# Kernel optimization log

Measured on AMD Instinct MI355X. Metric: run time of the kernel, lower is better.

The kernel has to match this reference:

```python
import jax, jax.numpy as jnp
import numpy as np

N_NODES = 100000
N_EDGES = 3200000
D_IN = 256
D_OUT = 256


def setup_inputs() -> dict:
    key = jax.random.key(0)
    k1, k2, k3, k4, k5 = jax.random.split(key, 5)
    inputs = jax.random.normal(k1, (N_NODES, D_IN), dtype=jnp.float32)
    # Glorot-uniform init as in _glorot_init
    init_range = np.sqrt(6.0 / (D_IN + D_OUT)).astype(np.float32)
    weight = jax.random.uniform(k2, (D_IN, D_OUT), dtype=jnp.float32,
                                minval=-init_range, maxval=init_range)
    edge_src = jax.random.randint(k3, (N_EDGES,), 0, N_NODES, dtype=jnp.int32)
    edge_dst = jax.random.randint(k4, (N_EDGES,), 0, N_NODES, dtype=jnp.int32)
    # normalized adjacency values (positive, like D^-1/2 A D^-1/2 entries)
    edge_vals = jax.random.uniform(k5, (N_EDGES,), dtype=jnp.float32)
    return {"inputs": inputs, "weight": weight, "edge_src": edge_src,
            "edge_dst": edge_dst, "edge_vals": edge_vals}


def reference(inputs, weight, edge_src, edge_dst, edge_vals):
    # x = inputs @ W          : [N, D_OUT]
    x = inputs @ weight
    # SpMM: out[d] = sum_{e: dst(e)=d} vals[e] * x[src(e)]
    msgs = edge_vals[:, None] * x[edge_src]          # [E, D_OUT]
    out = jax.ops.segment_sum(msgs, edge_dst, num_segments=inputs.shape[0])
    return jax.nn.relu(out)
```

## Files before the change

kernel.cpp:

```cpp
#include <hip/hip_runtime.h>

#define N_NODES 100000
#define N_EDGES 3200000
#define DDIM 256
#define NB 1563
#define BIN_BLK 256
#define CHUNK (N_EDGES / BIN_BLK)

typedef short s16x8 __attribute__((ext_vector_type(8)));
typedef float f32x4 __attribute__((ext_vector_type(4)));

__device__ __forceinline__ unsigned short f32_to_bf16(float f) {
    union { float f; unsigned int u; } c; c.f = f;
    unsigned int u = c.u;
    unsigned int r = u + 0x7fffu + ((u >> 16) & 1u);
    return (unsigned short)(r >> 16);
}
__device__ __forceinline__ float bf16_to_f32(unsigned short h) {
    union { unsigned int u; float f; } c; c.u = ((unsigned int)h) << 16;
    return c.f;
}

__global__ __launch_bounds__(256) void prep_w(const float* __restrict__ W,
                                              unsigned short* __restrict__ Wt) {
    __shared__ float tile[32][33];
    const int tx = threadIdx.x & 31;
    const int ty = threadIdx.x >> 5;
    const int n0 = blockIdx.x * 32;
    const int k0 = blockIdx.y * 32;
    for (int i = 0; i < 32; i += 8)
        tile[ty + i][tx] = W[(size_t)(k0 + ty + i) * DDIM + n0 + tx];
    __syncthreads();
    for (int i = 0; i < 32; i += 8)
        Wt[(size_t)(n0 + ty + i) * DDIM + k0 + tx] = f32_to_bf16(tile[tx][ty + i]);
}

__global__ __launch_bounds__(256) void gemm_mfma(const float* __restrict__ A,
                                                 const unsigned short* __restrict__ Wt,
                                                 unsigned short* __restrict__ Xb) {
    __shared__ unsigned short As[64][DDIM + 8];
    const int tid = threadIdx.x;
    const int rowBase = blockIdx.x * 64;

#pragma unroll
    for (int p = 0; p < 16; ++p) {
        const int flat = p * 256 + tid;
        const int row = flat >> 6;
        const int k4 = (flat & 63) * 4;
        const int gr = rowBase + row;
        float4 v = make_float4(0.f, 0.f, 0.f, 0.f);
        if (gr < N_NODES) v = *(const float4*)&A[(size_t)gr * DDIM + k4];
        ushort4 h;
        h.x = f32_to_bf16(v.x); h.y = f32_to_bf16(v.y);
        h.z = f32_to_bf16(v.z); h.w = f32_to_bf16(v.w);
        *(ushort4*)&As[row][k4] = h;
    }
    __syncthreads();

    const int wave = tid >> 6;
    const int lane = tid & 63;
    const int lrow = lane & 15;
    const int quad = lane >> 4;
    const int cb = wave * 64;

    f32x4 acc[4][4] = {};

#pragma unroll
    for (int ks = 0; ks < 8; ++ks) {
        const int k0 = ks * 32 + quad * 8;
        s16x8 a[4], b[4];
#pragma unroll
        for (int ri = 0; ri < 4; ++ri)
            a[ri] = *(const s16x8*)&As[ri * 16 + lrow][k0];
#pragma unroll
        for (int ci = 0; ci < 4; ++ci)
            b[ci] = *(const s16x8*)&Wt[(size_t)(cb + ci * 16 + lrow) * DDIM + k0];
#pragma unroll
        for (int ri = 0; ri < 4; ++ri)
#pragma unroll
            for (int ci = 0; ci < 4; ++ci)
                acc[ri][ci] = __builtin_amdgcn_mfma_f32_16x16x32_bf16(a[ri], b[ci], acc[ri][ci], 0, 0, 0);
    }

#pragma unroll
    for (int ri = 0; ri < 4; ++ri) {
        const int r0 = rowBase + ri * 16 + quad * 4;
#pragma unroll
        for (int rr = 0; rr < 4; ++rr) {
            const int row = r0 + rr;
            if (row < N_NODES) {
#pragma unroll
                for (int ci = 0; ci < 4; ++ci)
                    Xb[(size_t)row * DDIM + cb + ci * 16 + lrow] = f32_to_bf16(acc[ri][ci][rr]);
            }
        }
    }
}

__global__ __launch_bounds__(256) void hist_coarse(const int* __restrict__ edst,
                                                   int* __restrict__ gcounts) {
    __shared__ int h[NB];
    const int tid = threadIdx.x;
    for (int i = tid; i < NB; i += 256) h[i] = 0;
    __syncthreads();
    const int lo = blockIdx.x * CHUNK;
    const int hi = lo + CHUNK;
    for (int e = lo + tid; e < hi; e += 256) atomicAdd(&h[edst[e] >> 6], 1);
    __syncthreads();
    for (int i = tid; i < NB; i += 256)
        if (h[i]) atomicAdd(&gcounts[i], h[i]);
}

__global__ __launch_bounds__(256) void scan_coarse(const int* __restrict__ gcounts,
                                                   int* __restrict__ bbase,
                                                   int* __restrict__ bcursor,
                                                   int* __restrict__ off) {
    __shared__ int part[256];
    const int t = threadIdx.x;
    const int chunk = (NB + 255) / 256;
    const int lo = t * chunk;
    const int hi = min(lo + chunk, NB);
    int s = 0;
    for (int i = lo; i < hi; ++i) s += gcounts[i];
    part[t] = s;
    __syncthreads();
    for (int d = 1; d < 256; d <<= 1) {
        int a = (t >= d) ? part[t - d] : 0;
        __syncthreads();
        part[t] += a;
        __syncthreads();
    }
    int run = part[t] - s;
    for (int i = lo; i < hi; ++i) {
        bbase[i] = run;
        bcursor[i] = run;
        run += gcounts[i];
    }
    if (t == 255) {
        bbase[NB] = run;
        off[N_NODES] = run;
    }
}

__global__ __launch_bounds__(256) void bin_coarse(const int* __restrict__ esrc,
                                                  const int* __restrict__ edst,
                                                  const float* __restrict__ evals,
                                                  int* __restrict__ bcursor,
                                                  long long* __restrict__ tmp) {
    __shared__ int h[NB];
    __shared__ int sb[NB];
    const int tid = threadIdx.x;
    for (int i = tid; i < NB; i += 256) h[i] = 0;
    __syncthreads();
    const int lo = blockIdx.x * CHUNK;
    const int hi = lo + CHUNK;
    for (int e = lo + tid; e < hi; e += 256) atomicAdd(&h[edst[e] >> 6], 1);
    __syncthreads();
    for (int i = tid; i < NB; i += 256)
        sb[i] = h[i] ? atomicAdd(&bcursor[i], h[i]) : 0;
    __syncthreads();
    for (int e = lo + tid; e < hi; e += 256) {
        const int d = edst[e];
        const int b = d >> 6;
        const int p = atomicAdd(&sb[b], 1);
        const unsigned int lo32 = (unsigned int)(esrc[e] | ((d & 63) << 17));
        const unsigned int hi32 = (unsigned int)__float_as_int(evals[e]);
        __builtin_nontemporal_store((long long)(((unsigned long long)hi32 << 32) | lo32), &tmp[p]);
    }
}

__global__ __launch_bounds__(256) void refine(const long long* __restrict__ tmp,
                                              const int* __restrict__ bbase,
                                              int* __restrict__ off,
                                              long long* __restrict__ srcval) {
    __shared__ int nh[64];
    __shared__ int nb[64];
    const int b = blockIdx.x;
    const int tid = threadIdx.x;
    const int base = bbase[b];
    const int cnt = bbase[b + 1] - base;
    const int n0 = b * 64;
    const int nn = min(64, N_NODES - n0);
    if (tid < 64) nh[tid] = 0;
    __syncthreads();
    for (int i = tid; i < cnt; i += 256) {
        const long long q = __builtin_nontemporal_load(&tmp[base + i]);
        atomicAdd(&nh[((int)(unsigned int)q) >> 17], 1);
    }
    __syncthreads();
    if (tid == 0) {
        int run = 0;
        for (int i = 0; i < 64; ++i) { nb[i] = run; run += nh[i]; }
    }
    __syncthreads();
    if (tid < nn) off[n0 + tid] = base + nb[tid];
    __syncthreads();
    for (int i = tid; i < cnt; i += 256) {
        const long long q = __builtin_nontemporal_load(&tmp[base + i]);
        const unsigned int lo32 = (unsigned int)q;
        const int dl = (int)(lo32 >> 17);
        const int p = atomicAdd(&nb[dl], 1);
        srcval[base + p] = (long long)((q & 0xFFFFFFFF00000000ull) | (lo32 & 0x1FFFF));
    }
}

__global__ __launch_bounds__(256) void spmm_gather(const unsigned short* __restrict__ xb,
                                                   const int* __restrict__ off,
                                                   const long long* __restrict__ srcval,
                                                   float* __restrict__ out) {
    const int node = blockIdx.x * 4 + (threadIdx.x >> 6);
    const int lane = threadIdx.x & 63;
    const int start = off[node];
    const int end = off[node + 1];

    float4 acc = make_float4(0.f, 0.f, 0.f, 0.f);

    for (int base = start; base < end; base += 64) {
        const int cnt = min(64, end - base);
        int s_l = 0;
        float v_l = 0.f;
        if (lane < cnt) {
            const long long q = __builtin_nontemporal_load(&srcval[base + lane]);
            s_l = (int)((unsigned int)q & 0x1FFFF);
            v_l = __int_as_float((int)(q >> 32));
        }
        int j = 0;
        for (; j + 4 <= cnt; j += 4) {
            const int s0 = __shfl(s_l, j + 0);
            const int s1 = __shfl(s_l, j + 1);
            const int s2 = __shfl(s_l, j + 2);
            const int s3 = __shfl(s_l, j + 3);
            const float v0 = __shfl(v_l, j + 0);
            const float v1 = __shfl(v_l, j + 1);
            const float v2 = __shfl(v_l, j + 2);
            const float v3 = __shfl(v_l, j + 3);
            const ushort4 h0 = *(const ushort4*)&xb[(size_t)s0 * DDIM + lane * 4];
            const ushort4 h1 = *(const ushort4*)&xb[(size_t)s1 * DDIM + lane * 4];
            const ushort4 h2 = *(const ushort4*)&xb[(size_t)s2 * DDIM + lane * 4];
            const ushort4 h3 = *(const ushort4*)&xb[(size_t)s3 * DDIM + lane * 4];
            acc.x += v0 * bf16_to_f32(h0.x); acc.y += v0 * bf16_to_f32(h0.y);
            acc.z += v0 * bf16_to_f32(h0.z); acc.w += v0 * bf16_to_f32(h0.w);
            acc.x += v1 * bf16_to_f32(h1.x); acc.y += v1 * bf16_to_f32(h1.y);
            acc.z += v1 * bf16_to_f32(h1.z); acc.w += v1 * bf16_to_f32(h1.w);
            acc.x += v2 * bf16_to_f32(h2.x); acc.y += v2 * bf16_to_f32(h2.y);
            acc.z += v2 * bf16_to_f32(h2.z); acc.w += v2 * bf16_to_f32(h2.w);
            acc.x += v3 * bf16_to_f32(h3.x); acc.y += v3 * bf16_to_f32(h3.y);
            acc.z += v3 * bf16_to_f32(h3.z); acc.w += v3 * bf16_to_f32(h3.w);
        }
        for (; j < cnt; ++j) {
            const int s = __shfl(s_l, j);
            const float v = __shfl(v_l, j);
            const ushort4 h = *(const ushort4*)&xb[(size_t)s * DDIM + lane * 4];
            acc.x += v * bf16_to_f32(h.x); acc.y += v * bf16_to_f32(h.y);
            acc.z += v * bf16_to_f32(h.z); acc.w += v * bf16_to_f32(h.w);
        }
    }

    f32x4 o;
    o[0] = fmaxf(acc.x, 0.f);
    o[1] = fmaxf(acc.y, 0.f);
    o[2] = fmaxf(acc.z, 0.f);
    o[3] = fmaxf(acc.w, 0.f);
    __builtin_nontemporal_store(o, (f32x4*)&out[(size_t)node * DDIM + lane * 4]);
}

extern "C" void kernel_launch(void* const* d_in, const int* in_sizes, int n_in,
                              void* d_out, int out_size, void* d_ws, size_t ws_size,
                              hipStream_t stream) {
    const float* inputs = (const float*)d_in[0];
    const float* weight = (const float*)d_in[1];
    const int* esrc     = (const int*)d_in[2];
    const int* edst     = (const int*)d_in[3];
    const float* evals  = (const float*)d_in[4];
    float* out = (float*)d_out;

    unsigned short* xb = (unsigned short*)d_ws;
    unsigned short* Wt = xb + (size_t)N_NODES * DDIM;
    int* off     = (int*)(Wt + DDIM * DDIM);
    int* gcounts = off + N_NODES + 1;
    int* bbase   = gcounts + NB;
    int* bcursor = bbase + NB + 1;
    uintptr_t a  = ((uintptr_t)(bcursor + NB) + 15) & ~(uintptr_t)15;
    long long* tmp    = (long long*)a;
    long long* srcval = tmp + N_EDGES;

    prep_w<<<dim3(8, 8), 256, 0, stream>>>(weight, Wt);

    gemm_mfma<<<(N_NODES + 63) / 64, 256, 0, stream>>>(inputs, Wt, xb);

    (void)hipMemsetAsync(gcounts, 0, NB * sizeof(int), stream);
    hist_coarse<<<BIN_BLK, 256, 0, stream>>>(edst, gcounts);
    scan_coarse<<<1, 256, 0, stream>>>(gcounts, bbase, bcursor, off);
    bin_coarse<<<BIN_BLK, 256, 0, stream>>>(esrc, edst, evals, bcursor, tmp);
    refine<<<NB, 256, 0, stream>>>(tmp, bbase, off, srcval);

    spmm_gather<<<N_NODES / 4, 256, 0, stream>>>(xb, off, srcval, out);
}
```

Before: 659.8 us.

## Split SpMM gather into two column-half passes and drop nontemporal tmp accesses

Splits the SpMM gather into two launches, each covering 128 output columns. Each lane now loads 4 bytes per edge instead of 8, and the inner loop is unrolled to 8 edges. The aim is to halve the working set of the gathered x rows per pass so it fits better in cache (L2/MALL), at the cost of reading the CSR index/value stream twice. It also switches the tmp scatter and refine loads from nontemporal to regular accesses so the binned data can stay cached between kernels.

```diff
diff --git a/kernel.cpp b/kernel.cpp
--- a/kernel.cpp
+++ b/kernel.cpp
@@ -9,6 +9,7 @@
 
 typedef short s16x8 __attribute__((ext_vector_type(8)));
 typedef float f32x4 __attribute__((ext_vector_type(4)));
+typedef float f32x2 __attribute__((ext_vector_type(2)));
 
 __device__ __forceinline__ unsigned short f32_to_bf16(float f) {
     union { float f; unsigned int u; } c; c.f = f;
@@ -16,9 +17,11 @@
     unsigned int r = u + 0x7fffu + ((u >> 16) & 1u);
     return (unsigned short)(r >> 16);
 }
-__device__ __forceinline__ float bf16_to_f32(unsigned short h) {
-    union { unsigned int u; float f; } c; c.u = ((unsigned int)h) << 16;
-    return c.f;
+__device__ __forceinline__ float bl16(unsigned int u) {
+    union { unsigned int x; float f; } c; c.x = u << 16; return c.f;
+}
+__device__ __forceinline__ float bh16(unsigned int u) {
+    union { unsigned int x; float f; } c; c.x = u & 0xffff0000u; return c.f;
 }
 
 __global__ __launch_bounds__(256) void prep_w(const float* __restrict__ W,
@@ -165,7 +168,7 @@
         const int p = atomicAdd(&sb[b], 1);
         const unsigned int lo32 = (unsigned int)(esrc[e] | ((d & 63) << 17));
         const unsigned int hi32 = (unsigned int)__float_as_int(evals[e]);
-        __builtin_nontemporal_store((long long)(((unsigned long long)hi32 << 32) | lo32), &tmp[p]);
+        tmp[p] = (long long)(((unsigned long long)hi32 << 32) | lo32);
     }
 }
 
@@ -184,7 +187,7 @@
     if (tid < 64) nh[tid] = 0;
     __syncthreads();
     for (int i = tid; i < cnt; i += 256) {
-        const long long q = __builtin_nontemporal_load(&tmp[base + i]);
+        const long long q = tmp[base + i];
         atomicAdd(&nh[((int)(unsigned int)q) >> 17], 1);
     }
     __syncthreads();
@@ -196,7 +199,7 @@
     if (tid < nn) off[n0 + tid] = base + nb[tid];
     __syncthreads();
     for (int i = tid; i < cnt; i += 256) {
-        const long long q = __builtin_nontemporal_load(&tmp[base + i]);
+        const long long q = tmp[base + i];
         const unsigned int lo32 = (unsigned int)q;
         const int dl = (int)(lo32 >> 17);
         const int p = atomicAdd(&nb[dl], 1);
@@ -204,16 +207,19 @@
     }
 }
 
-__global__ __launch_bounds__(256) void spmm_gather(const unsigned short* __restrict__ xb,
-                                                   const int* __restrict__ off,
-                                                   const long long* __restrict__ srcval,
-                                                   float* __restrict__ out) {
+#define HEDGE(q) { a0 += v##q * bl16(h##q); a1 += v##q * bh16(h##q); }
+
+__global__ __launch_bounds__(256) void spmm_half(const unsigned short* __restrict__ xbh,
+                                                 const int* __restrict__ off,
+                                                 const long long* __restrict__ srcval,
+                                                 float* __restrict__ outh) {
     const int node = blockIdx.x * 4 + (threadIdx.x >> 6);
     const int lane = threadIdx.x & 63;
     const int start = off[node];
     const int end = off[node + 1];
 
-    float4 acc = make_float4(0.f, 0.f, 0.f, 0.f);
+    const unsigned short* xcol = xbh + lane * 2;
+    float a0 = 0.f, a1 = 0.f;
 
     for (int base = start; base < end; base += 64) {
         const int cnt = min(64, end - base);
@@ -225,44 +231,48 @@
             v_l = __int_as_float((int)(q >> 32));
         }
         int j = 0;
-        for (; j + 4 <= cnt; j += 4) {
+        for (; j + 8 <= cnt; j += 8) {
             const int s0 = __shfl(s_l, j + 0);
             const int s1 = __shfl(s_l, j + 1);
             const int s2 = __shfl(s_l, j + 2);
             const int s3 = __shfl(s_l, j + 3);
+            const int s4 = __shfl(s_l, j + 4);
+            const int s5 = __shfl(s_l, j + 5);
+            const int s6 = __shfl(s_l, j + 6);
+            const int s7 = __shfl(s_l, j + 7);
             const float v0 = __shfl(v_l, j + 0);
             const float v1 = __shfl(v_l, j + 1);
             const float v2 = __shfl(v_l, j + 2);
             const float v3 = __shfl(v_l, j + 3);
-            const ushort4 h0 = *(const ushort4*)&xb[(size_t)s0 * DDIM + lane * 4];
-            const ushort4 h1 = *(const ushort4*)&xb[(size_t)s1 * DDIM + lane * 4];
-            const ushort4 h2 = *(const ushort4*)&xb[(size_t)s2 * DDIM + lane * 4];
-            const ushort4 h3 = *(const ushort4*)&xb[(size_t)s3 * DDIM + lane * 4];
-            acc.x += v0 * bf16_to_f32(h0.x); acc.y += v0 * bf16_to_f32(h0.y);
-            acc.z += v0 * bf16_to_f32(h0.z); acc.w += v0 * bf16_to_f32(h0.w);
-            acc.x += v1 * bf16_to_f32(h1.x); acc.y += v1 * bf16_to_f32(h1.y);
-            acc.z += v1 * bf16_to_f32(h1.z); acc.w += v1 * bf16_to_f32(h1.w);
-            acc.x += v2 * bf16_to_f32(h2.x); acc.y += v2 * bf16_to_f32(h2.y);
-            acc.z += v2 * bf16_to_f32(h2.z); acc.w += v2 * bf16_to_f32(h2.w);
-            acc.x += v3 * bf16_to_f32(h3.x); acc.y += v3 * bf16_to_f32(h3.y);
-            acc.z += v3 * bf16_to_f32(h3.z); acc.w += v3 * bf16_to_f32(h3.w);
+            const float v4 = __shfl(v_l, j + 4);
+            const float v5 = __shfl(v_l, j + 5);
+            const float v6 = __shfl(v_l, j + 6);
+            const float v7 = __shfl(v_l, j + 7);
+            const unsigned int h0 = *(const unsigned int*)&xcol[(size_t)s0 * DDIM];
+            const unsigned int h1 = *(const unsigned int*)&xcol[(size_t)s1 * DDIM];
+            const unsigned int h2 = *(const unsigned int*)&xcol[(size_t)s2 * DDIM];
+            const unsigned int h3 = *(const unsigned int*)&xcol[(size_t)s3 * DDIM];
+            const unsigned int h4 = *(const unsigned int*)&xcol[(size_t)s4 * DDIM];
+            const unsigned int h5 = *(const unsigned int*)&xcol[(size_t)s5 * DDIM];
+            const unsigned int h6 = *(const unsigned int*)&xcol[(size_t)s6 * DDIM];
+            const unsigned int h7 = *(const unsigned int*)&xcol[(size_t)s7 * DDIM];
+            HEDGE(0) HEDGE(1) HEDGE(2) HEDGE(3)
+            HEDGE(4) HEDGE(5) HEDGE(6) HEDGE(7)
         }
         for (; j < cnt; ++j) {
             const int s = __shfl(s_l, j);
             const float v = __shfl(v_l, j);
-            const ushort4 h = *(const ushort4*)&xb[(size_t)s * DDIM + lane * 4];
-            acc.x += v * bf16_to_f32(h.x); acc.y += v * bf16_to_f32(h.y);
-            acc.z += v * bf16_to_f32(h.z); acc.w += v * bf16_to_f32(h.w);
+            const unsigned int h = *(const unsigned int*)&xcol[(size_t)s * DDIM];
+            a0 += v * bl16(h); a1 += v * bh16(h);
         }
     }
 
-    f32x4 o;
-    o[0] = fmaxf(acc.x, 0.f);
-    o[1] = fmaxf(acc.y, 0.f);
-    o[2] = fmaxf(acc.z, 0.f);
-    o[3] = fmaxf(acc.w, 0.f);
-    __builtin_nontemporal_store(o, (f32x4*)&out[(size_t)node * DDIM + lane * 4]);
-}
+    f32x2 o;
+    o[0] = fmaxf(a0, 0.f);
+    o[1] = fmaxf(a1, 0.f);
+    __builtin_nontemporal_store(o, (f32x2*)&outh[(size_t)node * DDIM + lane * 2]);
+}
+#undef HEDGE
 
 extern "C" void kernel_launch(void* const* d_in, const int* in_sizes, int n_in,
                               void* d_out, int out_size, void* d_ws, size_t ws_size,
@@ -294,5 +304,6 @@
     bin_coarse<<<BIN_BLK, 256, 0, stream>>>(esrc, edst, evals, bcursor, tmp);
     refine<<<NB, 256, 0, stream>>>(tmp, bbase, off, srcval);
 
-    spmm_gather<<<N_NODES / 4, 256, 0, stream>>>(xb, off, srcval, out);
-}
+    spmm_half<<<N_NODES / 4, 256, 0, stream>>>(xb,       off, srcval, out);
+    spmm_half<<<N_NODES / 4, 256, 0, stream>>>(xb + 128, off, srcval, out + 128);
+}
```

Result: faster. 599.8 us (-9.1%).
